# Kernel tuning notes

Hardware: AMD Instinct MI355X
Metric: run time of the kernel (lower is better)

## Reference

```python
import jax, jax.numpy as jnp
import numpy as np

PC = 512      # proposal_channels == conv_channels
INCH = 512    # in_channels of branch
B = 8
T = 64        # pyramid level length (feat_t) at order=0
TF = 256      # frame_level_feature length (clip_length)
KERNELS = [8, 16, 8, 4, 2, 2, 2]  # ConPoolingKernal
CLC = 498     # feature_lastclass channels (CLC + 2 == 500)
GROUPS = 32


def _gn(x, gamma, beta):
    # GroupNorm(32, C) over [B, C, L]
    Bb, C, L = x.shape
    xg = x.reshape(Bb, GROUPS, C // GROUPS, L)
    m = xg.mean(axis=(2, 3), keepdims=True)
    v = xg.var(axis=(2, 3), keepdims=True)
    xn = ((xg - m) * jax.lax.rsqrt(v + 1e-5)).reshape(Bb, C, L)
    return xn * gamma[None, :, None] + beta[None, :, None]


def _c1(x, w, b):
    # Unit1D kernel_shape=1: pointwise conv
    return jnp.einsum('bct,oc->bot', x, w) + b[None, :, None]


def _bmp(feat, segs):
    # BoundaryMaxPooling: first C/2 channels max-pooled over segs[...,0:2],
    # second C/2 over segs[...,2:4] (inclusive integer ranges, clamped).
    Bb, C, L = feat.shape
    C2 = C // 2
    pos = jnp.arange(L)
    def pool(f, s, e):
        s = jnp.clip(s, 0, L - 1)
        e = jnp.maximum(jnp.clip(e, 0, L - 1), s)
        mask = (pos[None, None, :] >= s[..., None]) & (pos[None, None, :] <= e[..., None])  # [B,T,L]
        return jnp.max(jnp.where(mask[:, None], f[:, :, None, :], -jnp.inf), axis=-1)  # [B,C2,T]
    return jnp.concatenate([pool(feat[:, :C2], segs[..., 0], segs[..., 1]),
                            pool(feat[:, C2:], segs[..., 2], segs[..., 3])], axis=1)


def _anchor_gather(feat, anc, K):
    # Vectorized per-anchor clamp/slice + nearest F.interpolate(size=K):
    # src index for output k of a slice [l, r] is l + floor(k * (r - l + 1) / K).
    Bb, C, L = feat.shape
    left = jnp.clip(anc[..., 0], 0, L)
    right = jnp.clip(anc[..., 1], 0, L)
    valid = right > left                      # empty slices -> zeros (torch branch)
    seglen = right + 1 - left
    k = jnp.arange(K)
    idx = jnp.clip(left[..., None] + (k[None, None, :] * seglen[..., None]) // K, 0, L - 1)  # [B,T,K]
    g = jax.vmap(lambda f, ix: f[:, ix])(feat, idx)   # [B,C,T,K]
    return g * valid[:, None, :, None].astype(feat.dtype)


def setup_inputs() -> dict:
    key = jax.random.key(0)
    ks = jax.random.split(key, 16)
    f32 = jnp.float32
    s = 0.02
    def w(k, shape):
        return jax.random.normal(k, shape, f32) * s
    inp = {}
    inp['feature'] = jax.random.normal(ks[0], (B, INCH, T), f32)
    inp['frame_level_feature'] = jax.random.normal(ks[1], (B, PC, TF), f32)
    inp['segments'] = jax.random.randint(ks[2], (B, T, 4), 0, T).astype(jnp.int32)
    inp['frame_segments'] = jax.random.randint(ks[3], (B, T, 4), 0, TF).astype(jnp.int32)
    inp['feature_lastclass'] = jax.random.normal(ks[4], (B, CLC, T), f32)
    inp['anchor'] = jnp.sort(jax.random.randint(ks[5], (B, T, 2), 0, T), axis=-1).astype(jnp.int32)
    inp['frame_anchor'] = jnp.sort(jax.random.randint(ks[6], (B, T, 2), 0, TF), axis=-1).astype(jnp.int32)
    inp['order'] = 0
    inp['LocResult_feature'] = jax.random.normal(ks[7], (B, 2, T), f32)
    inp['w_cur'] = w(ks[8], (PC, INCH)); inp['b_cur'] = jnp.zeros((PC,), f32)
    inp['g_cur'] = jnp.ones((PC,), f32); inp['be_cur'] = jnp.zeros((PC,), f32)
    inp['w_lr'] = w(ks[9], (2 * PC, INCH)); inp['b_lr'] = jnp.zeros((2 * PC,), f32)
    inp['g_lr'] = jnp.ones((2 * PC,), f32); inp['be_lr'] = jnp.zeros((2 * PC,), f32)
    inp['w_roi'] = w(ks[10], (PC, PC)); inp['b_roi'] = jnp.zeros((PC,), f32)
    inp['g_roi'] = jnp.ones((PC,), f32); inp['be_roi'] = jnp.zeros((PC,), f32)
    K1 = KERNELS[1]; K0 = KERNELS[0]
    inp['w_cp'] = w(ks[11], (PC, 2 * PC, K1)); inp['b_cp'] = jnp.zeros((PC,), f32)
    inp['w_cp0'] = w(ks[12], (PC, PC, K0)); inp['b_cp0'] = jnp.zeros((PC,), f32)
    CIN = 6 * PC + 500
    inp['w_prop'] = w(ks[13], (INCH, CIN)); inp['b_prop'] = jnp.zeros((INCH,), f32)
    inp['g_prop'] = jnp.ones((INCH,), f32); inp['be_prop'] = jnp.zeros((INCH,), f32)
    return inp


def reference(feature, frame_level_feature, segments, frame_segments, feature_lastclass,
              anchor, frame_anchor, order, LocResult_feature,
              w_cur, b_cur, g_cur, be_cur, w_lr, b_lr, g_lr, be_lr,
              w_roi, b_roi, g_roi, be_roi, w_cp, b_cp, w_cp0, b_cp0,
              w_prop, b_prop, g_prop, be_prop):
    relu = jax.nn.relu
    fm_short = relu(_gn(_c1(feature, w_cur, b_cur), g_cur, be_cur))           # [B,PC,T]
    feat_lr = relu(_gn(_c1(feature, w_lr, b_lr), g_lr, be_lr))                # [B,2PC,T]
    prop_feature = _bmp(feat_lr, segments)                                    # [B,2PC,T]
    prop_roi = relu(_gn(_c1(_bmp(frame_level_feature, frame_segments), w_roi, b_roi), g_roi, be_roi))
    K1 = KERNELS[order + 1]
    K0 = KERNELS[0]
    g1 = _anchor_gather(feat_lr, anchor, K1)                                  # [B,2PC,T,K1]
    con_feature = jnp.einsum('bctk,ock->bot', g1, w_cp) + b_cp[None, :, None]  # valid conv K1->1
    g0 = _anchor_gather(frame_level_feature, frame_anchor, K0)                # [B,PC,T,K0]
    frame_con = jnp.einsum('bctk,ock->bot', g0, w_cp0) + b_cp0[None, :, None]
    prop_con = relu(_gn(_c1(frame_con, w_roi, b_roi), g_roi, be_roi))
    cat = jnp.concatenate([prop_roi, prop_feature, fm_short, feature_lastclass,
                           con_feature, prop_con, LocResult_feature], axis=1)  # [B,6PC+500,T]
    out = relu(_gn(_c1(cat, w_prop, b_prop), g_prop, be_prop))                # [B,INCH,T]
    return (out, feat_lr)
```

## Files before the change

### kernel.cpp

```cpp
#include <hip/hip_runtime.h>
#include <math.h>

#define BB 8
#define CATP 3584
#define CAT_REAL 3572

typedef __attribute__((ext_vector_type(8))) short short8;
typedef __attribute__((ext_vector_type(4))) float f32x4;

__device__ inline ushort f2bf(float f) {
  union { float f; unsigned u; } x;
  x.f = f;
  return (ushort)((x.u + 0x7FFFu + ((x.u >> 16) & 1u)) >> 16);
}
__device__ inline float bf2f(unsigned us) {
  union { unsigned u; float f; } x;
  x.u = us << 16;
  return x.f;
}

template <int Cin, int Kf>
__device__ void cpT_tile(const float* __restrict__ W, ushort* __restrict__ D,
                         int nt, int cc) {
  const int tid = threadIdx.x;
  const int j = tid >> 6, l4 = (tid >> 4) & 3, l15 = tid & 15;
  const int o = nt * 64 + j * 16 + l15;
  const int cb = cc * 32 + l4 * 8;
  ushort rg[8][Kf];
#pragma unroll
  for (int q = 0; q < 8; q++) {
    const float* row = W + ((size_t)o * Cin + cb + q) * Kf;
#pragma unroll
    for (int kq = 0; kq < Kf / 4; kq++) {
      const float4 f = *(const float4*)(row + kq * 4);
      rg[q][kq * 4 + 0] = f2bf(f.x);
      rg[q][kq * 4 + 1] = f2bf(f.y);
      rg[q][kq * 4 + 2] = f2bf(f.z);
      rg[q][kq * 4 + 3] = f2bf(f.w);
    }
  }
#pragma unroll
  for (int k = 0; k < Kf; k++) {
    uint4 pk;
    pk.x = (unsigned)rg[0][k] | ((unsigned)rg[1][k] << 16);
    pk.y = (unsigned)rg[2][k] | ((unsigned)rg[3][k] << 16);
    pk.z = (unsigned)rg[4][k] | ((unsigned)rg[5][k] << 16);
    pk.w = (unsigned)rg[6][k] | ((unsigned)rg[7][k] << 16);
    *(uint4*)(D + ((size_t)(nt * Kf + k) * (Cin >> 5) + cc) * 2048 + tid * 8) = pk;
  }
}

__global__ __launch_bounds__(256) void prep_kernel(
    const float* __restrict__ w_cur, const float* __restrict__ w_lr,
    const float* __restrict__ w_roi, const float* __restrict__ w_prop,
    ushort* __restrict__ Wcomb, ushort* __restrict__ Wroi,
    ushort* __restrict__ Wprop, const float* __restrict__ w_cp,
    ushort* __restrict__ WcpT, const float* __restrict__ w_cp0,
    ushort* __restrict__ Wcp0T, const float* __restrict__ feature,
    const float* __restrict__ frame_feat, const float* __restrict__ lastcls,
    const float* __restrict__ locres, ushort* __restrict__ Ft,
    ushort* __restrict__ FfT, ushort* __restrict__ cat) {
  __shared__ float tile[64 * 65];
  const int bid = blockIdx.x;
  if (bid < 1408) {
    const int i = bid * 256 + threadIdx.x;
    const float* src;
    ushort* dst;
    int o, k8, Kc;
    bool pad = false;
    if (i < 98304) {
      o = i >> 6; k8 = i & 63; Kc = 16;
      src = (o < 512) ? (w_cur + (size_t)o * 512)
                      : (w_lr + (size_t)(o - 512) * 512);
      dst = Wcomb;
    } else if (i < 131072) {
      const int r = i - 98304;
      o = r >> 6; k8 = r & 63; Kc = 16;
      src = w_roi + (size_t)o * 512;
      dst = Wroi;
    } else {
      const int r = i - 131072;
      if (r >= 229376) return;
      o = r / 448; k8 = r % 448; Kc = 112;
      src = w_prop + (size_t)o * CAT_REAL;
      dst = Wprop;
      pad = true;
    }
    const int k = k8 * 8;
    float v[8];
    if (pad) {
#pragma unroll
      for (int q = 0; q < 8; q++) v[q] = (k + q < CAT_REAL) ? src[k + q] : 0.f;
    } else {
      const float4 f0 = *(const float4*)(src + k);
      const float4 f1 = *(const float4*)(src + k + 4);
      v[0] = f0.x; v[1] = f0.y; v[2] = f0.z; v[3] = f0.w;
      v[4] = f1.x; v[5] = f1.y; v[6] = f1.z; v[7] = f1.w;
    }
    uint4 pk;
    pk.x = (unsigned)f2bf(v[0]) | ((unsigned)f2bf(v[1]) << 16);
    pk.y = (unsigned)f2bf(v[2]) | ((unsigned)f2bf(v[3]) << 16);
    pk.z = (unsigned)f2bf(v[4]) | ((unsigned)f2bf(v[5]) << 16);
    pk.w = (unsigned)f2bf(v[6]) | ((unsigned)f2bf(v[7]) << 16);
    const int ot = o >> 6, ii = (o >> 4) & 3, l15 = o & 15;
    const int kc = k8 >> 2, l4 = k8 & 3;
    const size_t flat =
        ((((size_t)ot * Kc + kc) * 4 + ii) * 64 + l4 * 16 + l15) * 8;
    *(uint4*)(dst + flat) = pk;
    return;
  }
  if (bid < 1792) {
    const int local = bid - 1408;
    if (local < 256)
      cpT_tile<1024, 16>(w_cp, WcpT, local >> 5, local & 31);
    else {
      const int r = local - 256;
      cpT_tile<512, 8>(w_cp0, Wcp0T, r >> 4, r & 15);
    }
    return;
  }
  const int local = bid - 1792;
  const float* src;
  ushort* dst;
  int Cr, Cw, L, rs, co, cblk, lblk, b;
  if (local < 64) {
    src = feature; dst = Ft; Cr = 512; Cw = 512; L = 64; rs = 512; co = 0;
    cblk = local & 7; lblk = 0; b = local >> 3;
  } else if (local < 320) {
    const int r = local - 64;
    src = frame_feat; dst = FfT; Cr = 512; Cw = 512; L = 256; rs = 512; co = 0;
    cblk = r & 7; lblk = (r >> 3) & 3; b = r >> 5;
  } else if (local < 384) {
    const int r = local - 320;
    src = lastcls; dst = cat; Cr = 498; Cw = 498; L = 64; rs = CATP; co = 2048;
    cblk = r & 7; lblk = 0; b = r >> 3;
  } else {
    const int r = local - 384;
    src = locres; dst = cat; Cr = 2; Cw = 14; L = 64; rs = CATP; co = 3570;
    cblk = 0; lblk = 0; b = r;
  }
  const int c0 = cblk * 64, l0 = lblk * 64;
  for (int e = threadIdx.x; e < 4096; e += 256) {
    const int cc = e >> 6, ll = e & 63;
    const int c = c0 + cc;
    tile[cc * 65 + ll] = (c < Cr) ? src[((size_t)b * Cr + c) * L + l0 + ll] : 0.f;
  }
  __syncthreads();
  for (int e = threadIdx.x; e < 4096; e += 256) {
    const int ll = e >> 6, cc = e & 63;
    const int c = c0 + cc;
    if (c < Cw)
      dst[((size_t)b * L + l0 + ll) * rs + co + c] = f2bf(tile[cc * 65 + ll]);
  }
}

__device__ void gemm_gn_body(const ushort* __restrict__ Xt,
                             const ushort* __restrict__ Wb,
                             const float* __restrict__ bias,
                             const float* __restrict__ gamma,
                             const float* __restrict__ beta, int Kp,
                             int cpgShift, float* __restrict__ outF, int outFM,
                             ushort* __restrict__ catOut, int catStride,
                             int chOff, int ot, int b, float* smem) {
  float* red = smem;
  float* rs = smem + 4224;
  float* rss = smem + 4228;
  float* gmean = smem + 4232;
  float* grstd = smem + 4236;
  const int w = threadIdx.x >> 6;
  const int lane = threadIdx.x & 63;
  const int l15 = lane & 15, l4 = lane >> 4;
  const int o0 = ot * 64;

  f32x4 acc[4] = {};
  const ushort* wbase = Wb + (size_t)ot * (Kp >> 5) * 2048 + lane * 8;
  const ushort* bp[4];
#pragma unroll
  for (int j = 0; j < 4; j++)
    bp[j] = Xt + (size_t)(b * 64 + j * 16 + l15) * Kp + l4 * 8;
  const int nkc = Kp >> 5;
  for (int kc = 0; kc < nkc; kc++) {
    const short8 a = *(const short8*)(wbase + ((size_t)kc * 4 + w) * 512);
    short8 x[4];
#pragma unroll
    for (int j = 0; j < 4; j++) x[j] = *(const short8*)(bp[j] + kc * 32);
#pragma unroll
    for (int j = 0; j < 4; j++)
      acc[j] = __builtin_amdgcn_mfma_f32_16x16x32_bf16(a, x[j], acc[j], 0, 0, 0);
  }
#pragma unroll
  for (int j = 0; j < 4; j++)
#pragma unroll
    for (int r = 0; r < 4; r++) {
      const int m = w * 16 + l4 * 4 + r;
      red[m * 65 + j * 16 + l15] = acc[j][r] + bias[o0 + m];
    }
  __syncthreads();

  const int cpg = 1 << cpgShift;
  const int ngroups = 64 >> cpgShift;
  for (int gi = 0; gi < ngroups; gi++) {
    float s = 0.f, ss = 0.f;
    const int nel = cpg << 6;
    for (int e = threadIdx.x; e < nel; e += 256) {
      const float v = red[((gi << cpgShift) + (e >> 6)) * 65 + (e & 63)];
      s += v;
      ss += v * v;
    }
#pragma unroll
    for (int off = 32; off > 0; off >>= 1) {
      s += __shfl_down(s, off);
      ss += __shfl_down(ss, off);
    }
    if (lane == 0) { rs[w] = s; rss[w] = ss; }
    __syncthreads();
    if (threadIdx.x == 0) {
      const float ts = rs[0] + rs[1] + rs[2] + rs[3];
      const float tss = rss[0] + rss[1] + rss[2] + rss[3];
      const float mean = ts / (float)nel;
      const float var = tss / (float)nel - mean * mean;
      gmean[gi] = mean;
      grstd[gi] = rsqrtf(var + 1e-5f);
    }
    __syncthreads();
  }

  if (outF) {
    for (int e = threadIdx.x; e < 4096; e += 256) {
      const int m = e >> 6, n = e & 63;
      const int gi = m >> cpgShift;
      const int c = o0 + m;
      float v = (red[m * 65 + n] - gmean[gi]) * grstd[gi] * gamma[c] + beta[c];
      v = fmaxf(v, 0.f);
      outF[((size_t)b * outFM + c) * 64 + n] = v;
    }
  }
  if (catOut) {
    for (int e = threadIdx.x; e < 4096; e += 256) {
      const int n = e >> 6, m = e & 63;
      const int gi = m >> cpgShift;
      const int c = o0 + m;
      float v = (red[m * 65 + n] - gmean[gi]) * grstd[gi] * gamma[c] + beta[c];
      v = fmaxf(v, 0.f);
      catOut[((size_t)(b * 64) + n) * catStride + chOff + c] = f2bf(v);
    }
  }
}

__device__ void gemm_part_body(const ushort* __restrict__ Xt,
                               const ushort* __restrict__ Wb,
                               float* __restrict__ P, int ot, int b, int slice,
                               int kbeg, int kend) {
  const int w = threadIdx.x >> 6;
  const int lane = threadIdx.x & 63;
  const int l15 = lane & 15, l4 = lane >> 4;
  f32x4 acc[4] = {};
  const ushort* wbase = Wb + (size_t)ot * (CATP >> 5) * 2048 + lane * 8;
  const ushort* bp[4];
#pragma unroll
  for (int j = 0; j < 4; j++)
    bp[j] = Xt + (size_t)(b * 64 + j * 16 + l15) * CATP + l4 * 8;
  for (int k = kbeg; k < kend; k += 32) {
    const int kc = k >> 5;
    const short8 a = *(const short8*)(wbase + ((size_t)kc * 4 + w) * 512);
    short8 x[4];
#pragma unroll
    for (int j = 0; j < 4; j++) x[j] = *(const short8*)(bp[j] + k);
#pragma unroll
    for (int j = 0; j < 4; j++)
      acc[j] = __builtin_amdgcn_mfma_f32_16x16x32_bf16(a, x[j], acc[j], 0, 0, 0);
  }
  float* Pp = P + (((size_t)slice * BB + b) * 512 + ot * 64) * 64;
#pragma unroll
  for (int j = 0; j < 4; j++)
#pragma unroll
    for (int r = 0; r < 4; r++)
      Pp[(w * 16 + l4 * 4 + r) * 64 + j * 16 + l15] = acc[j][r];
}

__global__ __launch_bounds__(256) void reduce_gn_kernel(
    const ushort* __restrict__ cat, const ushort* __restrict__ Wprop,
    const float* __restrict__ P, const float* __restrict__ bias,
    const float* __restrict__ gamma, const float* __restrict__ beta,
    float* __restrict__ outF) {
  const int ot = blockIdx.x;
  const int b = blockIdx.y;
  const int o0 = ot * 64;
  const int w = threadIdx.x >> 6;
  const int lane = threadIdx.x & 63;
  const int l15 = lane & 15, l4 = lane >> 4;

  f32x4 acc[4] = {};
  const ushort* wbase = Wprop + (size_t)ot * (CATP >> 5) * 2048 + lane * 8;
  const ushort* bp[4];
#pragma unroll
  for (int j = 0; j < 4; j++)
    bp[j] = cat + (size_t)(b * 64 + j * 16 + l15) * CATP + l4 * 8;
  for (int k = 2528; k < 3584; k += 32) {
    const int kc = k >> 5;
    const short8 a = *(const short8*)(wbase + ((size_t)kc * 4 + w) * 512);
    short8 x[4];
#pragma unroll
    for (int j = 0; j < 4; j++) x[j] = *(const short8*)(bp[j] + k);
#pragma unroll
    for (int j = 0; j < 4; j++)
      acc[j] = __builtin_amdgcn_mfma_f32_16x16x32_bf16(a, x[j], acc[j], 0, 0, 0);
  }

  __shared__ float red[64 * 65];
#pragma unroll
  for (int j = 0; j < 4; j++)
#pragma unroll
    for (int r = 0; r < 4; r++)
      red[(w * 16 + l4 * 4 + r) * 65 + j * 16 + l15] = acc[j][r];
  __syncthreads();
  for (int e = threadIdx.x; e < 4096; e += 256) {
    const int m = e >> 6, n = e & 63;
    float s = bias[o0 + m];
#pragma unroll
    for (int z = 0; z < 4; z++)
      s += P[(((size_t)z * BB + b) * 512 + o0 + m) * 64 + n];
    red[m * 65 + n] += s;
  }
  __syncthreads();
  __shared__ float rs[4], rss[4], gmean[4], grstd[4];
  for (int gi = 0; gi < 4; gi++) {
    float s = 0.f, ss = 0.f;
    for (int e = threadIdx.x; e < 1024; e += 256) {
      const float v = red[((gi << 4) + (e >> 6)) * 65 + (e & 63)];
      s += v;
      ss += v * v;
    }
#pragma unroll
    for (int off = 32; off > 0; off >>= 1) {
      s += __shfl_down(s, off);
      ss += __shfl_down(ss, off);
    }
    if (lane == 0) { rs[w] = s; rss[w] = ss; }
    __syncthreads();
    if (threadIdx.x == 0) {
      const float ts = rs[0] + rs[1] + rs[2] + rs[3];
      const float tss = rss[0] + rss[1] + rss[2] + rss[3];
      const float mean = ts / 1024.f;
      const float var = tss / 1024.f - mean * mean;
      gmean[gi] = mean;
      grstd[gi] = rsqrtf(var + 1e-5f);
    }
    __syncthreads();
  }
  for (int e = threadIdx.x; e < 4096; e += 256) {
    const int m = e >> 6, n = e & 63;
    const int gi = m >> 4;
    const int c = o0 + m;
    float v = (red[m * 65 + n] - gmean[gi]) * grstd[gi] * gamma[c] + beta[c];
    outF[((size_t)b * 512 + c) * 64 + n] = fmaxf(v, 0.f);
  }
}

template <int C, int L>
__device__ void bmp_body(const ushort* __restrict__ Xt,
                         const int* __restrict__ segs, ushort* __restrict__ Y,
                         int rowStride, int chOff, int t, int b,
                         float2 (*pmax)[512]) {
  constexpr int C2 = C / 2;
  constexpr int P2 = C2 / 2;
  constexpr int CH = P2 / 64;
  const int w = threadIdx.x >> 6;
  const int lane = threadIdx.x & 63;
  const int* sg = segs + ((size_t)b * 64 + t) * 4;
  const ushort* Xb = Xt + (size_t)b * L * C;
#pragma unroll
  for (int h = 0; h < 2; h++) {
    const int s = min(max(sg[2 * h], 0), L - 1);
    const int e = max(min(max(sg[2 * h + 1], 0), L - 1), s);
#pragma unroll
    for (int q = 0; q < CH; q++) {
      const int p = q * 64 + lane;
      const ushort* base = Xb + h * C2 + 2 * p;
      float a0 = -INFINITY, a1 = -INFINITY;
      float c0 = -INFINITY, c1 = -INFINITY;
      int l = s + w;
      for (; l + 4 <= e; l += 8) {
        const unsigned u0 = *(const unsigned*)(base + (size_t)l * C);
        const unsigned u1 = *(const unsigned*)(base + (size_t)(l + 4) * C);
        a0 = fmaxf(a0, bf2f(u0 & 0xffffu));
        a1 = fmaxf(a1, bf2f(u0 >> 16));
        c0 = fmaxf(c0, bf2f(u1 & 0xffffu));
        c1 = fmaxf(c1, bf2f(u1 >> 16));
      }
      if (l <= e) {
        const unsigned u0 = *(const unsigned*)(base + (size_t)l * C);
        a0 = fmaxf(a0, bf2f(u0 & 0xffffu));
        a1 = fmaxf(a1, bf2f(u0 >> 16));
      }
      pmax[w][h * P2 + p] = make_float2(fmaxf(a0, c0), fmaxf(a1, c1));
    }
  }
  __syncthreads();
  for (int idx = threadIdx.x; idx < 2 * P2; idx += 256) {
    float2 m = pmax[0][idx];
#pragma unroll
    for (int ww = 1; ww < 4; ww++) {
      const float2 v = pmax[ww][idx];
      m.x = fmaxf(m.x, v.x);
      m.y = fmaxf(m.y, v.y);
    }
    const unsigned o = (unsigned)f2bf(m.x) | ((unsigned)f2bf(m.y) << 16);
    *(unsigned*)(Y + ((size_t)(b * 64) + t) * rowStride + chOff + 2 * idx) = o;
  }
}

template <int Kf, int L, int Cin, int NT, int CSPAN>
__device__ void anchor_body2(const ushort* __restrict__ src,
                             const int* __restrict__ anc,
                             const ushort* __restrict__ Wt,
                             float* __restrict__ P, int nt, int b, int tapbase,
                             int cbase, int slice) {
  const int w = threadIdx.x >> 6;
  const int lane = threadIdx.x & 63;
  const int l15 = lane & 15, l4 = lane >> 4;
  const int t = w * 16 + l15;
  const int a0 = anc[((size_t)b * 64 + t) * 2 + 0];
  const int a1 = anc[((size_t)b * 64 + t) * 2 + 1];
  const int left = min(max(a0, 0), L);
  const int right = min(max(a1, 0), L);
  const int seglen = right + 1 - left;

  f32x4 acc[4] = {};
#pragma unroll
  for (int kt = 0; kt < NT; kt++) {
    const int k = tapbase + kt;
    const int ix = min(max(left + (k * seglen) / Kf, 0), L - 1);
    const ushort* rp = src + ((size_t)b * L + ix) * Cin + cbase + l4 * 8;
    const ushort* wb = Wt + ((size_t)nt * Kf + k) * (Cin >> 5) * 2048 + lane * 8;
#pragma unroll 4
    for (int c0 = 0; c0 < CSPAN; c0 += 32) {
      const int cc = (cbase + c0) >> 5;
      const short8 a = *(const short8*)(rp + c0);
      short8 bbf[4];
#pragma unroll
      for (int j = 0; j < 4; j++)
        bbf[j] = *(const short8*)(wb + ((size_t)cc * 4 + j) * 512);
#pragma unroll
      for (int j = 0; j < 4; j++)
        acc[j] =
            __builtin_amdgcn_mfma_f32_16x16x32_bf16(a, bbf[j], acc[j], 0, 0, 0);
    }
  }
  float* Pp = P + (((size_t)slice * BB + b) * 64) * 512 + nt * 64;
#pragma unroll
  for (int j = 0; j < 4; j++)
#pragma unroll
    for (int r = 0; r < 4; r++)
      Pp[(size_t)(w * 16 + l4 * 4 + r) * 512 + j * 16 + l15] = acc[j][r];
}

__device__ void anchor_reduce_body(const float* __restrict__ P, int ks,
                                   const float* __restrict__ bias,
                                   const int* __restrict__ anc, int L,
                                   ushort* __restrict__ Y, int rowStride,
                                   int chOff, int ot, int b, float* smem) {
  float* tile = smem;
  float* sval = smem + 4160;
  const int o0 = ot * 64;
  if (threadIdx.x < 64) {
    const int t = threadIdx.x;
    const int a0 = anc[((size_t)b * 64 + t) * 2 + 0];
    const int a1 = anc[((size_t)b * 64 + t) * 2 + 1];
    const int left = min(max(a0, 0), L);
    const int right = min(max(a1, 0), L);
    sval[t] = (right > left) ? 1.f : 0.f;
  }
  __syncthreads();
  for (int e = threadIdx.x; e < 4096; e += 256) {
    const int m = e >> 6, nl = e & 63;
    float s = 0.f;
    for (int z = 0; z < ks; z++)
      s += P[(((size_t)z * BB + b) * 64 + m) * 512 + o0 + nl];
    tile[nl * 65 + m] = s * sval[m] + bias[o0 + nl];
  }
  __syncthreads();
  for (int e = threadIdx.x; e < 4096; e += 256) {
    const int m = e >> 6, nl = e & 63;
    Y[((size_t)(b * 64) + m) * rowStride + chOff + o0 + nl] =
        f2bf(tile[nl * 65 + m]);
  }
}

__global__ __launch_bounds__(256) void fused_B_kernel(
    const ushort* __restrict__ Ft, const ushort* __restrict__ Wcomb,
    const float* __restrict__ b_cur, const float* __restrict__ g_cur,
    const float* __restrict__ be_cur, ushort* __restrict__ cat,
    const float* __restrict__ b_lr, const float* __restrict__ g_lr,
    const float* __restrict__ be_lr, float* __restrict__ feat_lr,
    ushort* __restrict__ FlrT, const ushort* __restrict__ FfT,
    const int* __restrict__ frame_segs, ushort* __restrict__ XbmpT,
    const int* __restrict__ frame_anchor, const ushort* __restrict__ Wcp0T,
    float* __restrict__ P0) {
  __shared__ __align__(16) float smem[4240];
  const int bid = blockIdx.x;
  if (bid < 512) {
    const int nt = bid & 7, b = (bid >> 3) & 7, s = bid >> 6;
    anchor_body2<8, 256, 512, 1, 512>(FfT, frame_anchor, Wcp0T, P0, nt, b, s,
                                      0, s);
  } else if (bid < 704) {
    const int r = bid - 512;
    const int b = r / 24, ot24 = r % 24;
    if (ot24 < 8)
      gemm_gn_body(Ft, Wcomb, b_cur, g_cur, be_cur, 512, 4, nullptr, 0, cat,
                   CATP, 1536, ot24, b, smem);
    else
      gemm_gn_body(Ft, Wcomb + 512 * 512, b_lr, g_lr, be_lr, 512, 5, feat_lr,
                   1024, FlrT, 1024, 0, ot24 - 8, b, smem);
  } else {
    const int r = bid - 704;
    bmp_body<512, 256>(FfT, frame_segs, XbmpT, 512, 0, r & 63, r >> 6,
                       (float2(*)[512])smem);
  }
}

__global__ __launch_bounds__(256) void fused_C_kernel(
    const ushort* __restrict__ FlrT, const int* __restrict__ segments,
    ushort* __restrict__ cat, const int* __restrict__ anchor,
    const ushort* __restrict__ WcpT, float* __restrict__ P1,
    const float* __restrict__ P0, const float* __restrict__ b_cp0,
    const int* __restrict__ frame_anchor, ushort* __restrict__ FconT,
    const ushort* __restrict__ XbmpT, const ushort* __restrict__ Wroi,
    const float* __restrict__ b_roi, const float* __restrict__ g_roi,
    const float* __restrict__ be_roi) {
  __shared__ __align__(16) float smem[4240];
  const int bid = blockIdx.x;
  if (bid < 1024) {
    const int nt = bid & 7, b = (bid >> 3) & 7, s = bid >> 6;
    const int kz = s >> 1, ch = s & 1;
    anchor_body2<16, 64, 1024, 2, 512>(FlrT, anchor, WcpT, P1, nt, b, kz * 2,
                                       ch * 512, s);
  } else if (bid < 1088) {
    const int r = bid - 1024;
    gemm_gn_body(XbmpT, Wroi, b_roi, g_roi, be_roi, 512, 4, nullptr, 0, cat,
                 CATP, 0, r & 7, r >> 3, smem);
  } else if (bid < 1152) {
    const int r = bid - 1088;
    anchor_reduce_body(P0, 8, b_cp0, frame_anchor, 256, FconT, 512, 0, r & 7,
                       r >> 3, smem);
  } else {
    const int r = bid - 1152;
    bmp_body<1024, 64>(FlrT, segments, cat, CATP, 512, r & 63, r >> 6,
                       (float2(*)[512])smem);
  }
}

__global__ __launch_bounds__(256) void fused_D_kernel(
    const ushort* __restrict__ cat, const ushort* __restrict__ Wprop,
    float* __restrict__ P9, const float* __restrict__ P1,
    const float* __restrict__ b_cp, const int* __restrict__ anchor,
    ushort* __restrict__ catw, const ushort* __restrict__ FconT,
    const ushort* __restrict__ Wroi, const float* __restrict__ b_roi,
    const float* __restrict__ g_roi, const float* __restrict__ be_roi) {
  __shared__ __align__(16) float smem[4240];
  const int bid = blockIdx.x;
  if (bid < 256) {
    const int s = bid >> 6, q = bid & 63;
    const int kb = s * 640;
    const int ke = (s == 3) ? 2528 : kb + 640;
    gemm_part_body(cat, Wprop, P9, q & 7, q >> 3, s, kb, ke);
  } else if (bid < 320) {
    const int r = bid - 256;
    anchor_reduce_body(P1, 16, b_cp, anchor, 64, catw, CATP, 2546, r & 7,
                       r >> 3, smem);
  } else {
    const int r = bid - 320;
    gemm_gn_body(FconT, Wroi, b_roi, g_roi, be_roi, 512, 4, nullptr, 0, catw,
                 CATP, 3058, r & 7, r >> 3, smem);
  }
}

extern "C" void kernel_launch(void* const* d_in, const int* in_sizes, int n_in,
                              void* d_out, int out_size, void* d_ws,
                              size_t ws_size, hipStream_t stream) {
  const float* feature      = (const float*)d_in[0];
  const float* frame_feat   = (const float*)d_in[1];
  const int*   segments     = (const int*)d_in[2];
  const int*   frame_segs   = (const int*)d_in[3];
  const float* feat_lastcls = (const float*)d_in[4];
  const int*   anchor       = (const int*)d_in[5];
  const int*   frame_anchor = (const int*)d_in[6];
  const float* locres       = (const float*)d_in[8];
  const float* w_cur  = (const float*)d_in[9];
  const float* b_cur  = (const float*)d_in[10];
  const float* g_cur  = (const float*)d_in[11];
  const float* be_cur = (const float*)d_in[12];
  const float* w_lr   = (const float*)d_in[13];
  const float* b_lr   = (const float*)d_in[14];
  const float* g_lr   = (const float*)d_in[15];
  const float* be_lr  = (const float*)d_in[16];
  const float* w_roi  = (const float*)d_in[17];
  const float* b_roi  = (const float*)d_in[18];
  const float* g_roi  = (const float*)d_in[19];
  const float* be_roi = (const float*)d_in[20];
  const float* w_cp   = (const float*)d_in[21];
  const float* b_cp   = (const float*)d_in[22];
  const float* w_cp0  = (const float*)d_in[23];
  const float* b_cp0  = (const float*)d_in[24];
  const float* w_prop = (const float*)d_in[25];
  const float* b_prop = (const float*)d_in[26];
  const float* g_prop = (const float*)d_in[27];
  const float* be_prop= (const float*)d_in[28];

  float* out_main = (float*)d_out;
  float* feat_lr  = (float*)d_out + BB * 512 * 64;

  ushort* cat_t  = (ushort*)d_ws;
  ushort* Ft     = cat_t + 1835008;
  ushort* XbmpT  = Ft + 262144;
  ushort* FconT  = XbmpT + 262144;
  ushort* Wcomb  = FconT + 262144;
  ushort* Wroi   = Wcomb + 786432;
  ushort* Wprop  = Wroi + 262144;
  ushort* WcpT   = Wprop + 1835008;
  ushort* Wcp0T  = WcpT + 8388608;
  ushort* FlrT   = Wcp0T + 2097152;
  ushort* FfT    = FlrT + 524288;
  float*  P1     = (float*)(FfT + 1048576);
  float*  P0     = P1 + 4194304;
  float*  P9     = P0 + 2097152;

  prep_kernel<<<2184, 256, 0, stream>>>(
      w_cur, w_lr, w_roi, w_prop, Wcomb, Wroi, Wprop, w_cp, WcpT, w_cp0,
      Wcp0T, feature, frame_feat, feat_lastcls, locres, Ft, FfT, cat_t);

  fused_B_kernel<<<1216, 256, 0, stream>>>(
      Ft, Wcomb, b_cur, g_cur, be_cur, cat_t, b_lr, g_lr, be_lr, feat_lr,
      FlrT, FfT, frame_segs, XbmpT, frame_anchor, Wcp0T, P0);

  fused_C_kernel<<<1664, 256, 0, stream>>>(
      FlrT, segments, cat_t, anchor, WcpT, P1, P0, b_cp0, frame_anchor, FconT,
      XbmpT, Wroi, b_roi, g_roi, be_roi);

  fused_D_kernel<<<384, 256, 0, stream>>>(
      cat_t, Wprop, P9, P1, b_cp, anchor, cat_t, FconT, Wroi, b_roi, g_roi,
      be_roi);

  reduce_gn_kernel<<<dim3(8, BB), 256, 0, stream>>>(
      cat_t, Wprop, P9, b_prop, g_prop, be_prop, out_main);
}
```

Before: 298.2 us.

## Split K across waves with 4x4 MFMA register tiles and LDS reduction

Each GEMM-style body now has every wave compute the full 64x64 output tile over its own slice of K, holding a 4x4 block of MFMA accumulators. Previously each wave owned 16 rows over the whole K range. The per-wave partial sums are then combined through shared memory using serialized accumulation steps. The anchor conv bodies are restructured so each wave handles one tap with a full channel half, which halves the number of partial slices and blocks in the fused kernels, and the reduction consumers are adjusted to match. The aim is more reuse of loaded operands per MFMA and fewer partial-sum writes to global memory, at the cost of more accumulator registers, lower occupancy and extra barriers.

```diff
diff --git a/kernel.cpp b/kernel.cpp
--- a/kernel.cpp
+++ b/kernel.cpp
@@ -171,30 +171,50 @@
   const int lane = threadIdx.x & 63;
   const int l15 = lane & 15, l4 = lane >> 4;
   const int o0 = ot * 64;
-
-  f32x4 acc[4] = {};
+  const int wk = Kp >> 2;
+  const int kbeg = w * wk, kend = kbeg + wk;
+
+  f32x4 acc[4][4] = {};
   const ushort* wbase = Wb + (size_t)ot * (Kp >> 5) * 2048 + lane * 8;
   const ushort* bp[4];
 #pragma unroll
   for (int j = 0; j < 4; j++)
     bp[j] = Xt + (size_t)(b * 64 + j * 16 + l15) * Kp + l4 * 8;
-  const int nkc = Kp >> 5;
-  for (int kc = 0; kc < nkc; kc++) {
-    const short8 a = *(const short8*)(wbase + ((size_t)kc * 4 + w) * 512);
-    short8 x[4];
-#pragma unroll
-    for (int j = 0; j < 4; j++) x[j] = *(const short8*)(bp[j] + kc * 32);
-#pragma unroll
-    for (int j = 0; j < 4; j++)
-      acc[j] = __builtin_amdgcn_mfma_f32_16x16x32_bf16(a, x[j], acc[j], 0, 0, 0);
-  }
-#pragma unroll
-  for (int j = 0; j < 4; j++)
-#pragma unroll
-    for (int r = 0; r < 4; r++) {
-      const int m = w * 16 + l4 * 4 + r;
-      red[m * 65 + j * 16 + l15] = acc[j][r] + bias[o0 + m];
-    }
+
+  for (int k = kbeg; k < kend; k += 32) {
+    const int kc = k >> 5;
+    short8 a[4], x[4];
+#pragma unroll
+    for (int i = 0; i < 4; i++)
+      a[i] = *(const short8*)(wbase + ((size_t)kc * 4 + i) * 512);
+#pragma unroll
+    for (int j = 0; j < 4; j++) x[j] = *(const short8*)(bp[j] + k);
+#pragma unroll
+    for (int i = 0; i < 4; i++)
+#pragma unroll
+      for (int j = 0; j < 4; j++)
+        acc[i][j] = __builtin_amdgcn_mfma_f32_16x16x32_bf16(a[i], x[j],
+                                                            acc[i][j], 0, 0, 0);
+  }
+
+  for (int ww = 0; ww < 4; ww++) {
+    __syncthreads();
+    if (w == ww) {
+#pragma unroll
+      for (int i = 0; i < 4; i++)
+#pragma unroll
+        for (int j = 0; j < 4; j++)
+#pragma unroll
+          for (int r = 0; r < 4; r++) {
+            const int m = i * 16 + l4 * 4 + r;
+            const int n = j * 16 + l15;
+            if (ww == 0)
+              red[m * 65 + n] = acc[i][j][r] + bias[o0 + m];
+            else
+              red[m * 65 + n] += acc[i][j][r];
+          }
+    }
+  }
   __syncthreads();
 
   const int cpg = 1 << cpgShift;
@@ -250,32 +270,55 @@
 __device__ void gemm_part_body(const ushort* __restrict__ Xt,
                                const ushort* __restrict__ Wb,
                                float* __restrict__ P, int ot, int b, int slice,
-                               int kbeg, int kend) {
+                               int kc0, int kc1, float* red) {
   const int w = threadIdx.x >> 6;
   const int lane = threadIdx.x & 63;
   const int l15 = lane & 15, l4 = lane >> 4;
-  f32x4 acc[4] = {};
+
+  f32x4 acc[4][4] = {};
   const ushort* wbase = Wb + (size_t)ot * (CATP >> 5) * 2048 + lane * 8;
   const ushort* bp[4];
 #pragma unroll
   for (int j = 0; j < 4; j++)
     bp[j] = Xt + (size_t)(b * 64 + j * 16 + l15) * CATP + l4 * 8;
-  for (int k = kbeg; k < kend; k += 32) {
-    const int kc = k >> 5;
-    const short8 a = *(const short8*)(wbase + ((size_t)kc * 4 + w) * 512);
-    short8 x[4];
-#pragma unroll
-    for (int j = 0; j < 4; j++) x[j] = *(const short8*)(bp[j] + k);
-#pragma unroll
-    for (int j = 0; j < 4; j++)
-      acc[j] = __builtin_amdgcn_mfma_f32_16x16x32_bf16(a, x[j], acc[j], 0, 0, 0);
-  }
+
+  for (int kc = kc0 + w; kc < kc1; kc += 4) {
+    short8 a[4], x[4];
+#pragma unroll
+    for (int i = 0; i < 4; i++)
+      a[i] = *(const short8*)(wbase + ((size_t)kc * 4 + i) * 512);
+#pragma unroll
+    for (int j = 0; j < 4; j++) x[j] = *(const short8*)(bp[j] + kc * 32);
+#pragma unroll
+    for (int i = 0; i < 4; i++)
+#pragma unroll
+      for (int j = 0; j < 4; j++)
+        acc[i][j] = __builtin_amdgcn_mfma_f32_16x16x32_bf16(a[i], x[j],
+                                                            acc[i][j], 0, 0, 0);
+  }
+
+  for (int ww = 0; ww < 4; ww++) {
+    __syncthreads();
+    if (w == ww) {
+#pragma unroll
+      for (int i = 0; i < 4; i++)
+#pragma unroll
+        for (int j = 0; j < 4; j++)
+#pragma unroll
+          for (int r = 0; r < 4; r++) {
+            const int m = i * 16 + l4 * 4 + r;
+            const int n = j * 16 + l15;
+            if (ww == 0)
+              red[m * 65 + n] = acc[i][j][r];
+            else
+              red[m * 65 + n] += acc[i][j][r];
+          }
+    }
+  }
+  __syncthreads();
   float* Pp = P + (((size_t)slice * BB + b) * 512 + ot * 64) * 64;
-#pragma unroll
-  for (int j = 0; j < 4; j++)
-#pragma unroll
-    for (int r = 0; r < 4; r++)
-      Pp[(w * 16 + l4 * 4 + r) * 64 + j * 16 + l15] = acc[j][r];
+  for (int e = threadIdx.x; e < 4096; e += 256)
+    Pp[e] = red[(e >> 6) * 65 + (e & 63)];
 }
 
 __global__ __launch_bounds__(256) void reduce_gn_kernel(
@@ -290,35 +333,53 @@
   const int lane = threadIdx.x & 63;
   const int l15 = lane & 15, l4 = lane >> 4;
 
-  f32x4 acc[4] = {};
+  f32x4 acc[4][4] = {};
   const ushort* wbase = Wprop + (size_t)ot * (CATP >> 5) * 2048 + lane * 8;
   const ushort* bp[4];
 #pragma unroll
   for (int j = 0; j < 4; j++)
     bp[j] = cat + (size_t)(b * 64 + j * 16 + l15) * CATP + l4 * 8;
-  for (int k = 2528; k < 3584; k += 32) {
-    const int kc = k >> 5;
-    const short8 a = *(const short8*)(wbase + ((size_t)kc * 4 + w) * 512);
-    short8 x[4];
-#pragma unroll
-    for (int j = 0; j < 4; j++) x[j] = *(const short8*)(bp[j] + k);
-#pragma unroll
-    for (int j = 0; j < 4; j++)
-      acc[j] = __builtin_amdgcn_mfma_f32_16x16x32_bf16(a, x[j], acc[j], 0, 0, 0);
+
+  for (int kc = 79 + w; kc < 112; kc += 4) {
+    short8 a[4], x[4];
+#pragma unroll
+    for (int i = 0; i < 4; i++)
+      a[i] = *(const short8*)(wbase + ((size_t)kc * 4 + i) * 512);
+#pragma unroll
+    for (int j = 0; j < 4; j++) x[j] = *(const short8*)(bp[j] + kc * 32);
+#pragma unroll
+    for (int i = 0; i < 4; i++)
+#pragma unroll
+      for (int j = 0; j < 4; j++)
+        acc[i][j] = __builtin_amdgcn_mfma_f32_16x16x32_bf16(a[i], x[j],
+                                                            acc[i][j], 0, 0, 0);
   }
 
   __shared__ float red[64 * 65];
-#pragma unroll
-  for (int j = 0; j < 4; j++)
-#pragma unroll
-    for (int r = 0; r < 4; r++)
-      red[(w * 16 + l4 * 4 + r) * 65 + j * 16 + l15] = acc[j][r];
+  for (int ww = 0; ww < 4; ww++) {
+    __syncthreads();
+    if (w == ww) {
+#pragma unroll
+      for (int i = 0; i < 4; i++)
+#pragma unroll
+        for (int j = 0; j < 4; j++)
+#pragma unroll
+          for (int r = 0; r < 4; r++) {
+            const int m = i * 16 + l4 * 4 + r;
+            const int n = j * 16 + l15;
+            if (ww == 0)
+              red[m * 65 + n] = acc[i][j][r];
+            else
+              red[m * 65 + n] += acc[i][j][r];
+          }
+    }
+  }
   __syncthreads();
   for (int e = threadIdx.x; e < 4096; e += 256) {
     const int m = e >> 6, n = e & 63;
     float s = bias[o0 + m];
 #pragma unroll
-    for (int z = 0; z < 4; z++)
+    for (int z = 0; z < 3; z++)
       s += P[(((size_t)z * BB + b) * 512 + o0 + m) * 64 + n];
     red[m * 65 + n] += s;
   }
@@ -410,49 +471,74 @@
   }
 }
 
-template <int Kf, int L, int Cin, int NT, int CSPAN>
-__device__ void anchor_body2(const ushort* __restrict__ src,
-                             const int* __restrict__ anc,
-                             const ushort* __restrict__ Wt,
-                             float* __restrict__ P, int nt, int b, int tapbase,
-                             int cbase, int slice) {
+template <int Kf, int L, int Cin>
+__device__ void anchor_mfma_body(const ushort* __restrict__ src,
+                                 const int* __restrict__ anc,
+                                 const ushort* __restrict__ Wt,
+                                 float* __restrict__ P, int nt, int b,
+                                 int slice, float* red) {
   const int w = threadIdx.x >> 6;
   const int lane = threadIdx.x & 63;
   const int l15 = lane & 15, l4 = lane >> 4;
-  const int t = w * 16 + l15;
-  const int a0 = anc[((size_t)b * 64 + t) * 2 + 0];
-  const int a1 = anc[((size_t)b * 64 + t) * 2 + 1];
-  const int left = min(max(a0, 0), L);
-  const int right = min(max(a1, 0), L);
-  const int seglen = right + 1 - left;
-
-  f32x4 acc[4] = {};
-#pragma unroll
-  for (int kt = 0; kt < NT; kt++) {
-    const int k = tapbase + kt;
+  const int kz = slice >> 1, chalf = slice & 1;
+  const int k = kz * 4 + w;
+  const int cbase = chalf * (Cin / 2);
+
+  const ushort* rp[4];
+#pragma unroll
+  for (int i = 0; i < 4; i++) {
+    const int t = i * 16 + l15;
+    const int a0 = anc[((size_t)b * 64 + t) * 2 + 0];
+    const int a1 = anc[((size_t)b * 64 + t) * 2 + 1];
+    const int left = min(max(a0, 0), L);
+    const int right = min(max(a1, 0), L);
+    const int seglen = right + 1 - left;
     const int ix = min(max(left + (k * seglen) / Kf, 0), L - 1);
-    const ushort* rp = src + ((size_t)b * L + ix) * Cin + cbase + l4 * 8;
-    const ushort* wb = Wt + ((size_t)nt * Kf + k) * (Cin >> 5) * 2048 + lane * 8;
-#pragma unroll 4
-    for (int c0 = 0; c0 < CSPAN; c0 += 32) {
-      const int cc = (cbase + c0) >> 5;
-      const short8 a = *(const short8*)(rp + c0);
-      short8 bbf[4];
+    rp[i] = src + ((size_t)b * L + ix) * Cin + cbase + l4 * 8;
+  }
+  const ushort* wb = Wt + (size_t)(nt * Kf + k) * (Cin >> 5) * 2048 + lane * 8;
+
+  f32x4 acc[4][4] = {};
+  for (int c0 = 0; c0 < Cin / 2; c0 += 32) {
+    const int cc = (cbase + c0) >> 5;
+    short8 a[4], bb[4];
+#pragma unroll
+    for (int i = 0; i < 4; i++) a[i] = *(const short8*)(rp[i] + c0);
+#pragma unroll
+    for (int j = 0; j < 4; j++)
+      bb[j] = *(const short8*)(wb + ((size_t)cc * 4 + j) * 512);
+#pragma unroll
+    for (int i = 0; i < 4; i++)
 #pragma unroll
       for (int j = 0; j < 4; j++)
-        bbf[j] = *(const short8*)(wb + ((size_t)cc * 4 + j) * 512);
-#pragma unroll
-      for (int j = 0; j < 4; j++)
-        acc[j] =
-            __builtin_amdgcn_mfma_f32_16x16x32_bf16(a, bbf[j], acc[j], 0, 0, 0);
-    }
-  }
-  float* Pp = P + (((size_t)slice * BB + b) * 64) * 512 + nt * 64;
-#pragma unroll
-  for (int j = 0; j < 4; j++)
-#pragma unroll
-    for (int r = 0; r < 4; r++)
-      Pp[(size_t)(w * 16 + l4 * 4 + r) * 512 + j * 16 + l15] = acc[j][r];
+        acc[i][j] = __builtin_amdgcn_mfma_f32_16x16x32_bf16(a[i], bb[j],
+                                                            acc[i][j], 0, 0, 0);
+  }
+
+  for (int ww = 0; ww < 4; ww++) {
+    __syncthreads();
+    if (w == ww) {
+#pragma unroll
+      for (int i = 0; i < 4; i++)
+#pragma unroll
+        for (int j = 0; j < 4; j++)
+#pragma unroll
+          for (int r = 0; r < 4; r++) {
+            const int m = i * 16 + l4 * 4 + r;
+            const int n = j * 16 + l15;
+            if (ww == 0)
+              red[m * 65 + n] = acc[i][j][r];
+            else
+              red[m * 65 + n] += acc[i][j][r];
+          }
+    }
+  }
+  __syncthreads();
+  float* Pp = P + (((size_t)slice * BB + b) * 512 + nt * 64) * 64;
+  for (int e = threadIdx.x; e < 4096; e += 256) {
+    const int n = e >> 6, m = e & 63;
+    Pp[e] = red[m * 65 + n];
+  }
 }
 
 __device__ void anchor_reduce_body(const float* __restrict__ P, int ks,
@@ -473,11 +559,12 @@
   }
   __syncthreads();
   for (int e = threadIdx.x; e < 4096; e += 256) {
-    const int m = e >> 6, nl = e & 63;
+    const int nl = e >> 6, m = e & 63;
+    const int n = o0 + nl;
     float s = 0.f;
     for (int z = 0; z < ks; z++)
-      s += P[(((size_t)z * BB + b) * 64 + m) * 512 + o0 + nl];
-    tile[nl * 65 + m] = s * sval[m] + bias[o0 + nl];
+      s += P[(((size_t)z * BB + b) * 512 + n) * 64 + m];
+    tile[nl * 65 + m] = s * sval[m] + bias[n];
   }
   __syncthreads();
   for (int e = threadIdx.x; e < 4096; e += 256) {
@@ -499,12 +586,11 @@
     float* __restrict__ P0) {
   __shared__ __align__(16) float smem[4240];
   const int bid = blockIdx.x;
-  if (bid < 512) {
+  if (bid < 256) {
     const int nt = bid & 7, b = (bid >> 3) & 7, s = bid >> 6;
-    anchor_body2<8, 256, 512, 1, 512>(FfT, frame_anchor, Wcp0T, P0, nt, b, s,
-                                      0, s);
-  } else if (bid < 704) {
-    const int r = bid - 512;
+    anchor_mfma_body<8, 256, 512>(FfT, frame_anchor, Wcp0T, P0, nt, b, s, smem);
+  } else if (bid < 448) {
+    const int r = bid - 256;
     const int b = r / 24, ot24 = r % 24;
     if (ot24 < 8)
       gemm_gn_body(Ft, Wcomb, b_cur, g_cur, be_cur, 512, 4, nullptr, 0, cat,
@@ -513,7 +599,7 @@
       gemm_gn_body(Ft, Wcomb + 512 * 512, b_lr, g_lr, be_lr, 512, 5, feat_lr,
                    1024, FlrT, 1024, 0, ot24 - 8, b, smem);
   } else {
-    const int r = bid - 704;
+    const int r = bid - 448;
     bmp_body<512, 256>(FfT, frame_segs, XbmpT, 512, 0, r & 63, r >> 6,
                        (float2(*)[512])smem);
   }
@@ -530,21 +616,19 @@
     const float* __restrict__ be_roi) {
   __shared__ __align__(16) float smem[4240];
   const int bid = blockIdx.x;
-  if (bid < 1024) {
+  if (bid < 512) {
     const int nt = bid & 7, b = (bid >> 3) & 7, s = bid >> 6;
-    const int kz = s >> 1, ch = s & 1;
-    anchor_body2<16, 64, 1024, 2, 512>(FlrT, anchor, WcpT, P1, nt, b, kz * 2,
-                                       ch * 512, s);
-  } else if (bid < 1088) {
-    const int r = bid - 1024;
+    anchor_mfma_body<16, 64, 1024>(FlrT, anchor, WcpT, P1, nt, b, s, smem);
+  } else if (bid < 576) {
+    const int r = bid - 512;
     gemm_gn_body(XbmpT, Wroi, b_roi, g_roi, be_roi, 512, 4, nullptr, 0, cat,
                  CATP, 0, r & 7, r >> 3, smem);
-  } else if (bid < 1152) {
-    const int r = bid - 1088;
-    anchor_reduce_body(P0, 8, b_cp0, frame_anchor, 256, FconT, 512, 0, r & 7,
+  } else if (bid < 640) {
+    const int r = bid - 576;
+    anchor_reduce_body(P0, 4, b_cp0, frame_anchor, 256, FconT, 512, 0, r & 7,
                        r >> 3, smem);
   } else {
-    const int r = bid - 1152;
+    const int r = bid - 640;
     bmp_body<1024, 64>(FlrT, segments, cat, CATP, 512, r & 63, r >> 6,
                        (float2(*)[512])smem);
   }
@@ -559,17 +643,17 @@
     const float* __restrict__ g_roi, const float* __restrict__ be_roi) {
   __shared__ __align__(16) float smem[4240];
   const int bid = blockIdx.x;
-  if (bid < 256) {
+  if (bid < 192) {
     const int s = bid >> 6, q = bid & 63;
-    const int kb = s * 640;
-    const int ke = (s == 3) ? 2528 : kb + 640;
-    gemm_part_body(cat, Wprop, P9, q & 7, q >> 3, s, kb, ke);
-  } else if (bid < 320) {
-    const int r = bid - 256;
-    anchor_reduce_body(P1, 16, b_cp, anchor, 64, catw, CATP, 2546, r & 7,
+    const int kc0 = (s == 0) ? 0 : (s == 1) ? 27 : 53;
+    const int kc1 = (s == 0) ? 27 : (s == 1) ? 53 : 79;
+    gemm_part_body(cat, Wprop, P9, q & 7, q >> 3, s, kc0, kc1, smem);
+  } else if (bid < 256) {
+    const int r = bid - 192;
+    anchor_reduce_body(P1, 8, b_cp, anchor, 64, catw, CATP, 2546, r & 7,
                        r >> 3, smem);
   } else {
-    const int r = bid - 320;
+    const int r = bid - 256;
     gemm_gn_body(FconT, Wroi, b_roi, g_roi, be_roi, 512, 4, nullptr, 0, catw,
                  CATP, 3058, r & 7, r >> 3, smem);
   }
@@ -622,22 +706,22 @@
   ushort* FlrT   = Wcp0T + 2097152;
   ushort* FfT    = FlrT + 524288;
   float*  P1     = (float*)(FfT + 1048576);
-  float*  P0     = P1 + 4194304;
-  float*  P9     = P0 + 2097152;
+  float*  P0     = P1 + 2097152;
+  float*  P9     = P0 + 1048576;
 
   prep_kernel<<<2184, 256, 0, stream>>>(
       w_cur, w_lr, w_roi, w_prop, Wcomb, Wroi, Wprop, w_cp, WcpT, w_cp0,
       Wcp0T, feature, frame_feat, feat_lastcls, locres, Ft, FfT, cat_t);
 
-  fused_B_kernel<<<1216, 256, 0, stream>>>(
+  fused_B_kernel<<<960, 256, 0, stream>>>(
       Ft, Wcomb, b_cur, g_cur, be_cur, cat_t, b_lr, g_lr, be_lr, feat_lr,
       FlrT, FfT, frame_segs, XbmpT, frame_anchor, Wcp0T, P0);
 
-  fused_C_kernel<<<1664, 256, 0, stream>>>(
+  fused_C_kernel<<<1152, 256, 0, stream>>>(
       FlrT, segments, cat_t, anchor, WcpT, P1, P0, b_cp0, frame_anchor, FconT,
       XbmpT, Wroi, b_roi, g_roi, be_roi);
 
-  fused_D_kernel<<<384, 256, 0, stream>>>(
+  fused_D_kernel<<<320, 256, 0, stream>>>(
       cat_t, Wprop, P9, P1, b_cp, anchor, cat_t, FconT, Wroi, b_roi, g_roi,
       be_roi);
 
```

New measurement: 310.6 us. 4.2% more time.
